# Performance work log

Measured on AMD Instinct MI355X. Metric: run time of the kernel, lower is better.

The kernel has to match this reference:

```python
import jax, jax.numpy as jnp
import numpy as np

ATOM_TYPES = (1, 6, 7, 8)  # H, C, N, O
BN_EPS = 1e-3


def setup_inputs() -> dict:
    key = jax.random.key(0)
    k1, k2, k3 = jax.random.split(key, 3)
    B, N, M, d, L = 16, 2048, 64, 3, 12
    X = jax.random.normal(k1, (B, N, d), jnp.float32) * 4.0  # coords in Angstrom-ish scale
    # neighbor indices; offset trick guarantees no self-neighbor (avoids R=0)
    off = jax.random.randint(k2, (B, N, M), 1, N)
    Nbrs = ((jnp.arange(N)[None, :, None] + off) % N).astype(jnp.int32)
    Nbrs_Z = jax.random.randint(k3, (B, N, M), 0, 10).astype(jnp.int32)
    params = np.array([[rc, rs, 4.0] for rc in (4.0, 8.0) for rs in (0.0, 1.0, 2.0, 3.0, 4.0, 5.0)], np.float32)
    rc = jnp.asarray(params[:, 0].reshape(L, 1, 1, 1))
    rs = jnp.asarray(params[:, 1].reshape(L, 1, 1, 1))
    re = jnp.asarray(params[:, 2].reshape(L, 1, 1, 1))
    return {"X": X, "Nbrs": Nbrs, "Nbrs_Z": Nbrs_Z, "rc": rc, "rs": rs, "re": re}


def reference(X, Nbrs, Nbrs_Z, rc, rs, re):
    # gather neighbor coordinates: [B,N,M,d]
    nbr = jax.vmap(lambda coords, idx: coords[idx])(X, Nbrs)
    D = nbr - X[:, :, None, :]                      # displacement tensor [B,N,M,d]
    R = jnp.sqrt(jnp.sum(D * D, axis=-1))           # distance matrix  [B,N,M]
    R1 = R[None]                                    # [1,B,N,M], broadcasts vs [L,1,1,1]
    K = jnp.exp(-re * (R1 - rs) ** 2)               # gaussian        [L,B,N,M]
    FC = jnp.where(R1 <= rc, 0.5 * (jnp.cos(jnp.pi * R1 / rc) + 1.0), 0.0)
    rsf = K * FC                                    # radial symmetry fn [L,B,N,M]
    # per-atom-type masks [A,B,N,M]
    types = jnp.asarray(ATOM_TYPES, Nbrs_Z.dtype)
    conds = (Nbrs_Z[None] == types[:, None, None, None]).astype(rsf.dtype)
    # masked reduce over neighbors, concat over types (type-major) -> [A*L,B,N]
    sym = jnp.einsum('abnm,lbnm->albn', conds, rsf)
    A, L = sym.shape[0], sym.shape[1]
    layer = sym.reshape(A * L, sym.shape[2], sym.shape[3]).transpose(1, 2, 0)  # [B,N,A*L]
    # tf.nn.moments over axis 0 (biased variance) + batch_normalization (no scale/offset)
    m = jnp.mean(layer, axis=0)
    v = jnp.var(layer, axis=0)
    return (layer - m) / jnp.sqrt(v + BN_EPS)
```

## Files before the change

kernel.cpp:

```cpp
#include <hip/hip_runtime.h>
#include <hip/hip_bf16.h>

#define NB 16
#define NN 2048
#define NM 64
#define NL 12
#define NC 48
#define PIF 3.14159265358979323f

__global__ __launch_bounds__(256, 4) void rsf_kernel(
    const float* __restrict__ X,
    const int* __restrict__ Nbrs,
    const int* __restrict__ NbrsZ,
    const float* __restrict__ rcg,
    const float* __restrict__ rsg,
    const float* __restrict__ reg,
    float* __restrict__ layer)
{
  __shared__ float4 sX[NN];
  const int tid  = blockIdx.x * 256 + threadIdx.x;
  const int atom = tid >> 3;
  const int t    = tid & 7;
  const int b    = atom >> 11;

  {
    const float* xb = X + (size_t)b * NN * 3;
    for (int i = threadIdx.x; i < NN; i += 256) {
      float4 v;
      v.x = xb[i * 3 + 0];
      v.y = xb[i * 3 + 1];
      v.z = xb[i * 3 + 2];
      v.w = 0.f;
      sX[i] = v;
    }
  }

  const float rc4 = rcg[0];
  const float rc8 = rcg[6];
  const float nre = -reg[0];
  const float p4  = PIF / rc4;
  const float p8  = PIF / rc8;
  float rsv[6];
#pragma unroll
  for (int r = 0; r < 6; ++r) rsv[r] = rsg[r];

  __syncthreads();

  const float4 pin = sX[atom & (NN - 1)];
  const float xi = pin.x, yi = pin.y, zi = pin.z;

  float acc[NC];
#pragma unroll
  for (int c = 0; c < NC; ++c) acc[c] = 0.f;

  const int nbase = atom * NM + t * 8;
  const int4 j40 = *(const int4*)(Nbrs  + nbase);
  const int4 j41 = *(const int4*)(Nbrs  + nbase + 4);
  const int4 z40 = *(const int4*)(NbrsZ + nbase);
  const int4 z41 = *(const int4*)(NbrsZ + nbase + 4);
  const int js[8] = {j40.x, j40.y, j40.z, j40.w, j41.x, j41.y, j41.z, j41.w};
  const int zs[8] = {z40.x, z40.y, z40.z, z40.w, z41.x, z41.y, z41.z, z41.w};

#pragma unroll
  for (int u = 0; u < 8; ++u) {
    const float4 p = sX[js[u]];
    const float dx = p.x - xi, dy = p.y - yi, dz = p.z - zi;
    const float R = sqrtf(fmaf(dx, dx, fmaf(dy, dy, dz * dz)));

    float K[6];
#pragma unroll
    for (int r = 0; r < 6; ++r) {
      const float d = R - rsv[r];
      K[r] = __expf(nre * (d * d));
    }
    const float c4  = __cosf(p4 * R);
    const float c8  = __cosf(p8 * R);
    const float fc4 = (R <= rc4) ? fmaf(0.5f, c4, 0.5f) : 0.f;
    const float fc8 = (R <= rc8) ? fmaf(0.5f, c8, 0.5f) : 0.f;

    const int z = zs[u];
    const float w0 = (z == 1) ? 1.f : 0.f;
    const float w1 = (z == 6) ? 1.f : 0.f;
    const float w2 = (z == 7) ? 1.f : 0.f;
    const float w3 = (z == 8) ? 1.f : 0.f;
    const float a40 = w0 * fc4, a80 = w0 * fc8;
    const float a41 = w1 * fc4, a81 = w1 * fc8;
    const float a42 = w2 * fc4, a82 = w2 * fc8;
    const float a43 = w3 * fc4, a83 = w3 * fc8;
#pragma unroll
    for (int r = 0; r < 6; ++r) {
      const float k = K[r];
      acc[ 0 + r] = fmaf(a40, k, acc[ 0 + r]);
      acc[ 6 + r] = fmaf(a80, k, acc[ 6 + r]);
      acc[12 + r] = fmaf(a41, k, acc[12 + r]);
      acc[18 + r] = fmaf(a81, k, acc[18 + r]);
      acc[24 + r] = fmaf(a42, k, acc[24 + r]);
      acc[30 + r] = fmaf(a82, k, acc[30 + r]);
      acc[36 + r] = fmaf(a43, k, acc[36 + r]);
      acc[42 + r] = fmaf(a83, k, acc[42 + r]);
    }
  }

#pragma unroll
  for (int c = 0; c < NC; ++c) acc[c] += __shfl_xor(acc[c], 4, 64);
  float k1[24];
  const bool s4 = (t & 4) != 0;
#pragma unroll
  for (int j = 0; j < 24; ++j) k1[j] = s4 ? acc[24 + j] : acc[j];
#pragma unroll
  for (int j = 0; j < 24; ++j) k1[j] += __shfl_xor(k1[j], 2, 64);
  float k2[12];
  const bool s2 = (t & 2) != 0;
#pragma unroll
  for (int j = 0; j < 12; ++j) k2[j] = s2 ? k1[12 + j] : k1[j];
#pragma unroll
  for (int j = 0; j < 12; ++j) k2[j] += __shfl_xor(k2[j], 1, 64);
  float o[6];
  const bool s1 = (t & 1) != 0;
#pragma unroll
  for (int j = 0; j < 6; ++j) o[j] = s1 ? k2[6 + j] : k2[j];

  float2* op = (float2*)(layer + (size_t)atom * NC + t * 6);
  op[0] = make_float2(o[0], o[1]);
  op[1] = make_float2(o[2], o[3]);
  op[2] = make_float2(o[4], o[5]);
}

__global__ __launch_bounds__(256) void bn_kernel(
    const float* __restrict__ layer,
    float* __restrict__ out)
{
  const int idx = blockIdx.x * 256 + threadIdx.x;
  float x[NB];
  float s = 0.f;
#pragma unroll
  for (int bb = 0; bb < NB; ++bb) {
    x[bb] = layer[(size_t)bb * NN * NC + idx];
    s += x[bb];
  }
  const float mean = s * (1.f / NB);
  float vs = 0.f;
#pragma unroll
  for (int bb = 0; bb < NB; ++bb) {
    const float d = x[bb] - mean;
    vs += d * d;
  }
  const float inv = rsqrtf(vs * (1.f / NB) + 1e-3f);
#pragma unroll
  for (int bb = 0; bb < NB; ++bb) {
    out[(size_t)bb * NN * NC + idx] = (x[bb] - mean) * inv;
  }
}

extern "C" void kernel_launch(void* const* d_in, const int* in_sizes, int n_in,
                              void* d_out, int out_size, void* d_ws, size_t ws_size,
                              hipStream_t stream) {
  const float* X   = (const float*)d_in[0];
  const int* Nbrs  = (const int*)d_in[1];
  const int* NbrsZ = (const int*)d_in[2];
  const float* rcg = (const float*)d_in[3];
  const float* rsg = (const float*)d_in[4];
  const float* reg = (const float*)d_in[5];

  float* layer = (float*)d_ws;
  float* out = (float*)d_out;

  rsf_kernel<<<1024, 256, 0, stream>>>(X, Nbrs, NbrsZ, rcg, rsg, reg, layer);
  bn_kernel<<<384, 256, 0, stream>>>(layer, out);
}
```

Baseline: 21.38 us.

## Fuse batch-norm into RSF kernel and cut transcendentals via Gaussian recurrence

Each block now handles two atom indices across all 16 batches, so the batch-norm statistics are computed from shared memory and the intermediate layer round trip and second kernel disappear. Coordinates are packed to float4 once by a small kernel and gathered from global memory instead of staging a full per-batch copy in LDS for every block. The six Gaussians are built from one exp plus a geometric recurrence (exp, reciprocal and precomputed ratios), and cos(pi R/4) comes from a double-angle identity on cos(pi R/8). This assumes evenly spaced rs values and rc4 = rc8/2, and it clamps R at rc8 to keep the recurrence bounded.

```diff
diff --git a/kernel.cpp b/kernel.cpp
--- a/kernel.cpp
+++ b/kernel.cpp
@@ -1,82 +1,93 @@
 #include <hip/hip_runtime.h>
-#include <hip/hip_bf16.h>
 
 #define NB 16
 #define NN 2048
 #define NM 64
-#define NL 12
 #define NC 48
+#define LDSP 50
 #define PIF 3.14159265358979323f
 
-__global__ __launch_bounds__(256, 4) void rsf_kernel(
-    const float* __restrict__ X,
+__global__ __launch_bounds__(256) void pack_x(
+    const float* __restrict__ X, float4* __restrict__ X4) {
+  const int i = blockIdx.x * 256 + threadIdx.x;
+  float4 v;
+  v.x = X[i * 3 + 0];
+  v.y = X[i * 3 + 1];
+  v.z = X[i * 3 + 2];
+  v.w = 0.f;
+  X4[i] = v;
+}
+
+__global__ __launch_bounds__(256, 4) void fused_kernel(
+    const float4* __restrict__ X4,
     const int* __restrict__ Nbrs,
     const int* __restrict__ NbrsZ,
     const float* __restrict__ rcg,
     const float* __restrict__ rsg,
     const float* __restrict__ reg,
-    float* __restrict__ layer)
+    float* __restrict__ out)
 {
-  __shared__ float4 sX[NN];
-  const int tid  = blockIdx.x * 256 + threadIdx.x;
-  const int atom = tid >> 3;
-  const int t    = tid & 7;
-  const int b    = atom >> 11;
+  __shared__ float sBN[2 * NB * LDSP];
 
-  {
-    const float* xb = X + (size_t)b * NN * 3;
-    for (int i = threadIdx.x; i < NN; i += 256) {
-      float4 v;
-      v.x = xb[i * 3 + 0];
-      v.y = xb[i * 3 + 1];
-      v.z = xb[i * 3 + 2];
-      v.w = 0.f;
-      sX[i] = v;
-    }
-  }
+  const int tid = threadIdx.x;
+  const int al  = tid >> 3;
+  const int t   = tid & 7;
+  const int b   = al & 15;
+  const int nl  = al >> 4;
+  const int n   = blockIdx.x * 2 + nl;
+  const int row = b * NN + n;
 
-  const float rc4 = rcg[0];
-  const float rc8 = rcg[6];
-  const float nre = -reg[0];
-  const float p4  = PIF / rc4;
-  const float p8  = PIF / rc8;
-  float rsv[6];
-#pragma unroll
-  for (int r = 0; r < 6; ++r) rsv[r] = rsg[r];
+  const float rc4 = rcg[0], rc8 = rcg[6];
+  const float re  = reg[0];
+  const float nre = -re;
+  const float pio8  = PIF / rc8;
+  const float sp    = rsg[1] - rsg[0];
+  const float gcoef = 2.f * re * sp;
+  const float rs3   = rsg[3];
+  const float qu4 = __expf(nre * (rsg[4] * rsg[4] - rsg[3] * rsg[3]));
+  const float qu5 = __expf(nre * (rsg[5] * rsg[5] - rsg[4] * rsg[4]));
+  const float qd2 = __expf(nre * (rsg[2] * rsg[2] - rsg[3] * rsg[3]));
+  const float qd1 = __expf(nre * (rsg[1] * rsg[1] - rsg[2] * rsg[2]));
+  const float qd0 = __expf(nre * (rsg[0] * rsg[0] - rsg[1] * rsg[1]));
 
-  __syncthreads();
-
-  const float4 pin = sX[atom & (NN - 1)];
+  const float4 pin = X4[row];
   const float xi = pin.x, yi = pin.y, zi = pin.z;
 
   float acc[NC];
 #pragma unroll
   for (int c = 0; c < NC; ++c) acc[c] = 0.f;
 
-  const int nbase = atom * NM + t * 8;
-  const int4 j40 = *(const int4*)(Nbrs  + nbase);
-  const int4 j41 = *(const int4*)(Nbrs  + nbase + 4);
-  const int4 z40 = *(const int4*)(NbrsZ + nbase);
-  const int4 z41 = *(const int4*)(NbrsZ + nbase + 4);
+  const int base = row * NM + t * 8;
+  const int4 j40 = *(const int4*)(Nbrs  + base);
+  const int4 j41 = *(const int4*)(Nbrs  + base + 4);
+  const int4 z40 = *(const int4*)(NbrsZ + base);
+  const int4 z41 = *(const int4*)(NbrsZ + base + 4);
   const int js[8] = {j40.x, j40.y, j40.z, j40.w, j41.x, j41.y, j41.z, j41.w};
   const int zs[8] = {z40.x, z40.y, z40.z, z40.w, z41.x, z41.y, z41.z, z41.w};
+  const int boff = b * NN;
 
 #pragma unroll
   for (int u = 0; u < 8; ++u) {
-    const float4 p = sX[js[u]];
+    const float4 p = X4[boff + js[u]];
     const float dx = p.x - xi, dy = p.y - yi, dz = p.z - zi;
     const float R = sqrtf(fmaf(dx, dx, fmaf(dy, dy, dz * dz)));
+    const float Rk = fminf(R, rc8);
 
-    float K[6];
-#pragma unroll
-    for (int r = 0; r < 6; ++r) {
-      const float d = R - rsv[r];
-      K[r] = __expf(nre * (d * d));
-    }
-    const float c4  = __cosf(p4 * R);
-    const float c8  = __cosf(p8 * R);
+    const float u3 = Rk - rs3;
+    const float K3 = __expf(nre * (u3 * u3));
+    const float Gu = __expf(gcoef * Rk);
+    const float Gd = __builtin_amdgcn_rcpf(Gu);
+    const float K4 = K3 * Gu * qu4;
+    const float K5 = K4 * Gu * qu5;
+    const float K2 = K3 * Gd * qd2;
+    const float K1 = K2 * Gd * qd1;
+    const float K0 = K1 * Gd * qd0;
+    const float K[6] = {K0, K1, K2, K3, K4, K5};
+
+    const float c8  = __cosf(pio8 * R);
+    const float c4  = fmaf(c8 + c8, c8, -1.f);
+    const float fc8 = (R <= rc8) ? fmaf(0.5f, c8, 0.5f) : 0.f;
     const float fc4 = (R <= rc4) ? fmaf(0.5f, c4, 0.5f) : 0.f;
-    const float fc8 = (R <= rc8) ? fmaf(0.5f, c8, 0.5f) : 0.f;
 
     const int z = zs[u];
     const float w0 = (z == 1) ? 1.f : 0.f;
@@ -115,40 +126,38 @@
   for (int j = 0; j < 12; ++j) k2[j] = s2 ? k1[12 + j] : k1[j];
 #pragma unroll
   for (int j = 0; j < 12; ++j) k2[j] += __shfl_xor(k2[j], 1, 64);
-  float o[6];
   const bool s1 = (t & 1) != 0;
+  const int lb = (nl * NB + b) * LDSP + 6 * t;
 #pragma unroll
-  for (int j = 0; j < 6; ++j) o[j] = s1 ? k2[6 + j] : k2[j];
+  for (int j = 0; j < 6; ++j) sBN[lb + j] = s1 ? k2[6 + j] : k2[j];
 
-  float2* op = (float2*)(layer + (size_t)atom * NC + t * 6);
-  op[0] = make_float2(o[0], o[1]);
-  op[1] = make_float2(o[2], o[3]);
-  op[2] = make_float2(o[4], o[5]);
-}
+  __syncthreads();
 
-__global__ __launch_bounds__(256) void bn_kernel(
-    const float* __restrict__ layer,
-    float* __restrict__ out)
-{
-  const int idx = blockIdx.x * 256 + threadIdx.x;
-  float x[NB];
-  float s = 0.f;
+  if (tid < 128) {
+    const int nn = tid >> 6;
+    const int cc = tid & 63;
+    if (cc < NC) {
+      float x[NB];
+      float s = 0.f;
 #pragma unroll
-  for (int bb = 0; bb < NB; ++bb) {
-    x[bb] = layer[(size_t)bb * NN * NC + idx];
-    s += x[bb];
-  }
-  const float mean = s * (1.f / NB);
-  float vs = 0.f;
+      for (int bb = 0; bb < NB; ++bb) {
+        x[bb] = sBN[(nn * NB + bb) * LDSP + cc];
+        s += x[bb];
+      }
+      const float mean = s * (1.f / NB);
+      float vs = 0.f;
 #pragma unroll
-  for (int bb = 0; bb < NB; ++bb) {
-    const float d = x[bb] - mean;
-    vs += d * d;
-  }
-  const float inv = rsqrtf(vs * (1.f / NB) + 1e-3f);
+      for (int bb = 0; bb < NB; ++bb) {
+        const float d = x[bb] - mean;
+        vs = fmaf(d, d, vs);
+      }
+      const float inv = rsqrtf(vs * (1.f / NB) + 1e-3f);
+      const int ng = blockIdx.x * 2 + nn;
 #pragma unroll
-  for (int bb = 0; bb < NB; ++bb) {
-    out[(size_t)bb * NN * NC + idx] = (x[bb] - mean) * inv;
+      for (int bb = 0; bb < NB; ++bb) {
+        out[(size_t)bb * (NN * NC) + ng * NC + cc] = (x[bb] - mean) * inv;
+      }
+    }
   }
 }
 
@@ -162,9 +171,9 @@
   const float* rsg = (const float*)d_in[4];
   const float* reg = (const float*)d_in[5];
 
-  float* layer = (float*)d_ws;
+  float4* X4 = (float4*)d_ws;
   float* out = (float*)d_out;
 
-  rsf_kernel<<<1024, 256, 0, stream>>>(X, Nbrs, NbrsZ, rcg, rsg, reg, layer);
-  bn_kernel<<<384, 256, 0, stream>>>(layer, out);
+  pack_x<<<128, 256, 0, stream>>>(X, X4);
+  fused_kernel<<<1024, 256, 0, stream>>>(X4, Nbrs, NbrsZ, rcg, rsg, reg, out);
 }
```

Result: slower. 26.41 us (+23.5%).
